# Optimization experiments

Hardware: AMD Instinct MI355X
Metric: run time of the kernel (lower is better)

The kernel has to match this reference:

```python
import jax, jax.numpy as jnp
import numpy as np

NUM_CLASSES = 1000
DENSE_DIM = 64 * 64  # 4096, hardcoded in the module
BATCH = 8192
W0, W1 = 0.5, 0.5  # self.weights


def setup_inputs() -> dict:
    key = jax.random.key(0)
    k1, k2, k3, k4 = jax.random.split(key, 4)
    logits = jax.random.normal(k1, (BATCH, NUM_CLASSES), dtype=jnp.float32)
    dense_out = jax.random.normal(k2, (BATCH, DENSE_DIM), dtype=jnp.float32)
    target = jax.random.randint(k3, (BATCH,), 0, NUM_CLASSES, dtype=jnp.int32)
    # dense_labels buffer: random 0/1 per (class, dense) cell, as in __init__
    dense_labels = jax.random.bernoulli(k4, 0.5, (NUM_CLASSES, DENSE_DIM)).astype(jnp.float32)
    return {"logits": logits, "dense_out": dense_out, "target": target,
            "dense_labels": dense_labels}


def _bce_with_logits_mean(x, y):
    # numerically stable BCEWithLogitsLoss (mean reduction)
    return jnp.mean(jnp.maximum(x, 0.0) - x * y + jnp.log1p(jnp.exp(-jnp.abs(x))))


def reference(logits, dense_out, target, dense_labels):
    # --- accumulation (detached in the original; side-effect state) ---
    probs = jax.lax.stop_gradient(jax.nn.sigmoid(dense_out))  # [B, D]
    dense_output_sum = jax.ops.segment_sum(probs, target, num_segments=NUM_CLASSES)  # [C, D]
    total_accumulated = jax.ops.segment_sum(
        jnp.ones((BATCH,), dtype=jnp.float32), target, num_segments=NUM_CLASSES)  # [C]

    # --- losses ---
    dense_target = dense_labels[target]  # per-sample gather of label rows [B, D]
    logp = jax.nn.log_softmax(logits, axis=-1)
    loss1 = -jnp.mean(jnp.take_along_axis(logp, target[:, None], axis=1))  # CrossEntropyLoss
    loss2 = _bce_with_logits_mean(dense_out, dense_target)
    loss = loss1 * W0 + loss2 * W1
    return loss, dense_output_sum, total_accumulated
```

## Files before the change

### kernel.cpp

```cpp
#include <hip/hip_runtime.h>
#include <math.h>

#define NC   1000
#define DD   4096
#define BB   8192


__global__ __launch_bounds__(1024) void build_k(const int* __restrict__ target,
                                                int* __restrict__ counts_g,
                                                int* __restrict__ offsets_g,
                                                int* __restrict__ csr) {
    __shared__ int scnt[1024];
    __shared__ int scur[1024];
    int t = threadIdx.x;
    scnt[t] = 0;
    __syncthreads();

    int tg[8];
    #pragma unroll
    for (int k = 0; k < 8; ++k) {
        tg[k] = target[k * 1024 + t];
        atomicAdd(&scnt[tg[k]], 1);
    }
    __syncthreads();

    int orig = scnt[t];
    __syncthreads();
    for (int off = 1; off < 1024; off <<= 1) {
        int v = (t >= off) ? scnt[t - off] : 0;
        __syncthreads();
        scnt[t] += v;
        __syncthreads();
    }
    int excl = scnt[t] - orig;
    if (t < NC) { counts_g[t] = orig; offsets_g[t] = excl; }
    scur[t] = excl;
    __syncthreads();

    #pragma unroll
    for (int k = 0; k < 8; ++k) {
        int pos = atomicAdd(&scur[tg[k]], 1);
        csr[pos] = k * 1024 + t;
    }
}

__global__ __launch_bounds__(256) void ce_k(const float* __restrict__ logits,
                                            const int* __restrict__ target,
                                            double* __restrict__ loss1) {
    int wave = threadIdx.x >> 6;
    int lane = threadIdx.x & 63;
    int i = blockIdx.x * 4 + wave;
    const float* row = logits + (size_t)i * NC;
    int j0 = lane * 4;

    float4 r0 = *(const float4*)(row + j0);
    float4 r1 = *(const float4*)(row + j0 + 256);
    float4 r2 = *(const float4*)(row + j0 + 512);
    float4 r3;
    if (j0 + 768 < NC) r3 = *(const float4*)(row + j0 + 768);
    else r3 = make_float4(-INFINITY, -INFINITY, -INFINITY, -INFINITY);
    float tl = row[target[i]];

    float mx = fmaxf(fmaxf(fmaxf(r0.x, r0.y), fmaxf(r0.z, r0.w)),
                     fmaxf(fmaxf(r1.x, r1.y), fmaxf(r1.z, r1.w)));
    mx = fmaxf(mx, fmaxf(fmaxf(r2.x, r2.y), fmaxf(r2.z, r2.w)));
    mx = fmaxf(mx, fmaxf(fmaxf(r3.x, r3.y), fmaxf(r3.z, r3.w)));
    #pragma unroll
    for (int o = 32; o > 0; o >>= 1) mx = fmaxf(mx, __shfl_xor(mx, o));

    float s = __expf(r0.x - mx) + __expf(r0.y - mx) + __expf(r0.z - mx) + __expf(r0.w - mx)
            + __expf(r1.x - mx) + __expf(r1.y - mx) + __expf(r1.z - mx) + __expf(r1.w - mx)
            + __expf(r2.x - mx) + __expf(r2.y - mx) + __expf(r2.z - mx) + __expf(r2.w - mx)
            + __expf(r3.x - mx) + __expf(r3.y - mx) + __expf(r3.z - mx) + __expf(r3.w - mx);
    #pragma unroll
    for (int o = 32; o > 0; o >>= 1) s += __shfl_xor(s, o);

    __shared__ float red[4];
    if (lane == 0) red[wave] = -(tl - mx - __logf(s));
    __syncthreads();
    if (threadIdx.x == 0)
        atomicAdd(loss1, (double)(red[0] + red[1] + red[2] + red[3]));
}

#define ACC1(xv, yv, acc)                                                     \
    {                                                                         \
        float e = __expf(-fabsf(xv));                                         \
        float inv = __builtin_amdgcn_rcpf(1.f + e);                           \
        acc += (xv >= 0.f) ? inv : e * inv;                                   \
        bce += fmaxf(xv, 0.f) - xv * yv + __logf(1.f + e);                    \
    }

__global__ __launch_bounds__(256) void main_k(const float* __restrict__ dense_out,
                                              const float* __restrict__ dense_labels,
                                              const int* __restrict__ counts,
                                              const int* __restrict__ offsets,
                                              const int* __restrict__ csr,
                                              float* __restrict__ out_sum,
                                              double* __restrict__ loss2) {
    int c = blockIdx.x;
    int d = blockIdx.y * 1024 + (threadIdx.x << 2);
    int n = counts[c];
    int o = offsets[c];
    __shared__ int sidx[128];

    float4 y = *(const float4*)(dense_labels + (size_t)c * DD + d);
    float a0 = 0.f, a1 = 0.f, a2 = 0.f, a3 = 0.f, bce = 0.f;
    const float* dp = dense_out + d;

    for (int base = 0; base < n; base += 128) {
        int m = min(128, n - base);
        if (threadIdx.x < m) sidx[threadIdx.x] = csr[o + base + threadIdx.x];
        __syncthreads();

        float4 x0 = *(const float4*)(dp + (size_t)sidx[0] * DD);
        int s = 0;
        for (; s + 1 < m; ++s) {
            float4 x1 = *(const float4*)(dp + (size_t)sidx[s + 1] * DD);
            ACC1(x0.x, y.x, a0) ACC1(x0.y, y.y, a1)
            ACC1(x0.z, y.z, a2) ACC1(x0.w, y.w, a3)
            x0 = x1;
        }
        ACC1(x0.x, y.x, a0) ACC1(x0.y, y.y, a1)
        ACC1(x0.z, y.z, a2) ACC1(x0.w, y.w, a3)
        __syncthreads();
    }

    float* p = out_sum + (size_t)c * DD + d;
    p[0] = a0; p[1] = a1; p[2] = a2; p[3] = a3;

    #pragma unroll
    for (int o2 = 32; o2 > 0; o2 >>= 1) bce += __shfl_xor(bce, o2);
    __shared__ float wsum[4];
    int t = threadIdx.x;
    if ((t & 63) == 0) wsum[t >> 6] = bce;
    __syncthreads();
    if (t == 0) atomicAdd(loss2, (double)(wsum[0] + wsum[1] + wsum[2] + wsum[3]));
}

__global__ void fin_k(const int* __restrict__ counts,
                      const double* __restrict__ loss1,
                      const double* __restrict__ loss2,
                      float* __restrict__ out) {
    int t = blockIdx.x * blockDim.x + threadIdx.x;
    if (t < NC) out[1 + (size_t)NC * DD + t] = (float)counts[t];
    if (t == 0) {
        double l1 = *loss1 / (double)BB;
        double l2 = *loss2 / ((double)BB * (double)DD);
        out[0] = (float)(0.5 * l1 + 0.5 * l2);
    }
}

extern "C" void kernel_launch(void* const* d_in, const int* in_sizes, int n_in,
                              void* d_out, int out_size, void* d_ws, size_t ws_size,
                              hipStream_t stream) {
    const float* logits       = (const float*)d_in[0];
    const float* dense_out    = (const float*)d_in[1];
    const int*   target       = (const int*)d_in[2];
    const float* dense_labels = (const float*)d_in[3];
    float* out = (float*)d_out;

    char* ws = (char*)d_ws;
    double* loss1   = (double*)(ws + 0);
    double* loss2   = (double*)(ws + 8);
    int*    counts  = (int*)(ws + 16);
    int*    offsets = (int*)(ws + 4096);
    int*    csr     = (int*)(ws + 8192);

    hipMemsetAsync(d_ws, 0, 16, stream);

    build_k<<<1, 1024, 0, stream>>>(target, counts, offsets, csr);
    ce_k<<<BB / 4, 256, 0, stream>>>(logits, target, loss1);

    dim3 grid(NC, DD / 1024);
    main_k<<<grid, 256, 0, stream>>>(dense_out, dense_labels, counts, offsets, csr,
                                     out + 1, loss2);
    fin_k<<<(NC + 255) / 256, 256, 0, stream>>>(counts, loss1, loss2, out);
}
```

Before: 286.9 us.

## Fuse CSR build, cross-entropy, BCE and finalize into one kernel

Replaces the four-kernel pipeline with a single fused kernel. Each class block scans the whole target array itself to collect its sample indices in shared memory, so the serial single-block CSR build is gone. Cross-entropy blocks are appended to the same grid, and the last block to finish (tracked by an atomic counter) writes the final loss. This removes launch gaps and the serialized build step, but adds redundant reads of the target array per block and assumes at most 128 samples per class.

```diff
diff --git a/kernel.cpp b/kernel.cpp
--- a/kernel.cpp
+++ b/kernel.cpp
@@ -5,82 +5,11 @@
 #define DD   4096
 #define BB   8192
 
+#define MAIN_BLOCKS (NC * 4)
+#define CE_BLOCKS   (BB / 4)
+#define TOT_BLOCKS  (MAIN_BLOCKS + CE_BLOCKS)
+#define MAXN 128
 
-__global__ __launch_bounds__(1024) void build_k(const int* __restrict__ target,
-                                                int* __restrict__ counts_g,
-                                                int* __restrict__ offsets_g,
-                                                int* __restrict__ csr) {
-    __shared__ int scnt[1024];
-    __shared__ int scur[1024];
-    int t = threadIdx.x;
-    scnt[t] = 0;
-    __syncthreads();
-
-    int tg[8];
-    #pragma unroll
-    for (int k = 0; k < 8; ++k) {
-        tg[k] = target[k * 1024 + t];
-        atomicAdd(&scnt[tg[k]], 1);
-    }
-    __syncthreads();
-
-    int orig = scnt[t];
-    __syncthreads();
-    for (int off = 1; off < 1024; off <<= 1) {
-        int v = (t >= off) ? scnt[t - off] : 0;
-        __syncthreads();
-        scnt[t] += v;
-        __syncthreads();
-    }
-    int excl = scnt[t] - orig;
-    if (t < NC) { counts_g[t] = orig; offsets_g[t] = excl; }
-    scur[t] = excl;
-    __syncthreads();
-
-    #pragma unroll
-    for (int k = 0; k < 8; ++k) {
-        int pos = atomicAdd(&scur[tg[k]], 1);
-        csr[pos] = k * 1024 + t;
-    }
-}
-
-__global__ __launch_bounds__(256) void ce_k(const float* __restrict__ logits,
-                                            const int* __restrict__ target,
-                                            double* __restrict__ loss1) {
-    int wave = threadIdx.x >> 6;
-    int lane = threadIdx.x & 63;
-    int i = blockIdx.x * 4 + wave;
-    const float* row = logits + (size_t)i * NC;
-    int j0 = lane * 4;
-
-    float4 r0 = *(const float4*)(row + j0);
-    float4 r1 = *(const float4*)(row + j0 + 256);
-    float4 r2 = *(const float4*)(row + j0 + 512);
-    float4 r3;
-    if (j0 + 768 < NC) r3 = *(const float4*)(row + j0 + 768);
-    else r3 = make_float4(-INFINITY, -INFINITY, -INFINITY, -INFINITY);
-    float tl = row[target[i]];
-
-    float mx = fmaxf(fmaxf(fmaxf(r0.x, r0.y), fmaxf(r0.z, r0.w)),
-                     fmaxf(fmaxf(r1.x, r1.y), fmaxf(r1.z, r1.w)));
-    mx = fmaxf(mx, fmaxf(fmaxf(r2.x, r2.y), fmaxf(r2.z, r2.w)));
-    mx = fmaxf(mx, fmaxf(fmaxf(r3.x, r3.y), fmaxf(r3.z, r3.w)));
-    #pragma unroll
-    for (int o = 32; o > 0; o >>= 1) mx = fmaxf(mx, __shfl_xor(mx, o));
-
-    float s = __expf(r0.x - mx) + __expf(r0.y - mx) + __expf(r0.z - mx) + __expf(r0.w - mx)
-            + __expf(r1.x - mx) + __expf(r1.y - mx) + __expf(r1.z - mx) + __expf(r1.w - mx)
-            + __expf(r2.x - mx) + __expf(r2.y - mx) + __expf(r2.z - mx) + __expf(r2.w - mx)
-            + __expf(r3.x - mx) + __expf(r3.y - mx) + __expf(r3.z - mx) + __expf(r3.w - mx);
-    #pragma unroll
-    for (int o = 32; o > 0; o >>= 1) s += __shfl_xor(s, o);
-
-    __shared__ float red[4];
-    if (lane == 0) red[wave] = -(tl - mx - __logf(s));
-    __syncthreads();
-    if (threadIdx.x == 0)
-        atomicAdd(loss1, (double)(red[0] + red[1] + red[2] + red[3]));
-}
 
 #define ACC1(xv, yv, acc)                                                     \
     {                                                                         \
@@ -90,63 +19,118 @@
         bce += fmaxf(xv, 0.f) - xv * yv + __logf(1.f + e);                    \
     }
 
-__global__ __launch_bounds__(256) void main_k(const float* __restrict__ dense_out,
-                                              const float* __restrict__ dense_labels,
-                                              const int* __restrict__ counts,
-                                              const int* __restrict__ offsets,
-                                              const int* __restrict__ csr,
-                                              float* __restrict__ out_sum,
-                                              double* __restrict__ loss2) {
-    int c = blockIdx.x;
-    int d = blockIdx.y * 1024 + (threadIdx.x << 2);
-    int n = counts[c];
-    int o = offsets[c];
-    __shared__ int sidx[128];
+__global__ __launch_bounds__(256) void fused_k(const float* __restrict__ logits,
+                                               const float* __restrict__ dense_out,
+                                               const int*   __restrict__ target,
+                                               const float* __restrict__ dense_labels,
+                                               float* __restrict__ out,
+                                               double* __restrict__ loss1,
+                                               double* __restrict__ loss2,
+                                               unsigned* __restrict__ done) {
+    int bx = blockIdx.x;
+    int t  = threadIdx.x;
+    int wave = t >> 6;
+    int lane = t & 63;
 
-    float4 y = *(const float4*)(dense_labels + (size_t)c * DD + d);
-    float a0 = 0.f, a1 = 0.f, a2 = 0.f, a3 = 0.f, bce = 0.f;
-    const float* dp = dense_out + d;
+    __shared__ int   sidx[MAXN];
+    __shared__ int   s_n;
+    __shared__ float red[4];
 
-    for (int base = 0; base < n; base += 128) {
-        int m = min(128, n - base);
-        if (threadIdx.x < m) sidx[threadIdx.x] = csr[o + base + threadIdx.x];
+    if (bx < MAIN_BLOCKS) {
+        int c     = bx >> 2;
+        int chunk = bx & 3;
+        int d     = chunk * 1024 + (t << 2);
+
+        if (t == 0) s_n = 0;
         __syncthreads();
 
-        float4 x0 = *(const float4*)(dp + (size_t)sidx[0] * DD);
-        int s = 0;
-        for (; s + 1 < m; ++s) {
-            float4 x1 = *(const float4*)(dp + (size_t)sidx[s + 1] * DD);
+        const int4* tp = (const int4*)target;
+        #pragma unroll
+        for (int k = 0; k < 8; ++k) {
+            int4 v = tp[k * 256 + t];
+            int s0 = (k * 256 + t) * 4;
+            if (v.x == c) { int p = atomicAdd(&s_n, 1); sidx[p] = s0;     }
+            if (v.y == c) { int p = atomicAdd(&s_n, 1); sidx[p] = s0 + 1; }
+            if (v.z == c) { int p = atomicAdd(&s_n, 1); sidx[p] = s0 + 2; }
+            if (v.w == c) { int p = atomicAdd(&s_n, 1); sidx[p] = s0 + 3; }
+        }
+        __syncthreads();
+        int n = s_n;
+
+        float4 y = *(const float4*)(dense_labels + (size_t)c * DD + d);
+        float a0 = 0.f, a1 = 0.f, a2 = 0.f, a3 = 0.f, bce = 0.f;
+        const float* dp = dense_out + d;
+
+        if (n > 0) {
+            float4 x0 = *(const float4*)(dp + (size_t)sidx[0] * DD);
+            int s = 0;
+            for (; s + 1 < n; ++s) {
+                float4 x1 = *(const float4*)(dp + (size_t)sidx[s + 1] * DD);
+                ACC1(x0.x, y.x, a0) ACC1(x0.y, y.y, a1)
+                ACC1(x0.z, y.z, a2) ACC1(x0.w, y.w, a3)
+                x0 = x1;
+            }
             ACC1(x0.x, y.x, a0) ACC1(x0.y, y.y, a1)
             ACC1(x0.z, y.z, a2) ACC1(x0.w, y.w, a3)
-            x0 = x1;
         }
-        ACC1(x0.x, y.x, a0) ACC1(x0.y, y.y, a1)
-        ACC1(x0.z, y.z, a2) ACC1(x0.w, y.w, a3)
+
+        float* p = out + 1 + (size_t)c * DD + d;
+        p[0] = a0; p[1] = a1; p[2] = a2; p[3] = a3;
+
+        if (chunk == 0 && t == 0) out[1 + (size_t)NC * DD + c] = (float)n;
+
+        #pragma unroll
+        for (int o2 = 32; o2 > 0; o2 >>= 1) bce += __shfl_xor(bce, o2);
+        if (lane == 0) red[wave] = bce;
         __syncthreads();
+        if (t == 0)
+            atomicAdd(loss2, (double)(red[0] + red[1] + red[2] + red[3]));
+    } else {
+        int i = (bx - MAIN_BLOCKS) * 4 + wave;
+        const float* row = logits + (size_t)i * NC;
+        int j0 = lane * 4;
+
+        float4 r0 = *(const float4*)(row + j0);
+        float4 r1 = *(const float4*)(row + j0 + 256);
+        float4 r2 = *(const float4*)(row + j0 + 512);
+        float4 r3;
+        if (j0 + 768 < NC) r3 = *(const float4*)(row + j0 + 768);
+        else r3 = make_float4(-INFINITY, -INFINITY, -INFINITY, -INFINITY);
+        float tl = row[target[i]];
+
+        float mx = fmaxf(fmaxf(fmaxf(r0.x, r0.y), fmaxf(r0.z, r0.w)),
+                         fmaxf(fmaxf(r1.x, r1.y), fmaxf(r1.z, r1.w)));
+        mx = fmaxf(mx, fmaxf(fmaxf(r2.x, r2.y), fmaxf(r2.z, r2.w)));
+        mx = fmaxf(mx, fmaxf(fmaxf(r3.x, r3.y), fmaxf(r3.z, r3.w)));
+        #pragma unroll
+        for (int o = 32; o > 0; o >>= 1) mx = fmaxf(mx, __shfl_xor(mx, o));
+
+        float s = __expf(r0.x - mx) + __expf(r0.y - mx) + __expf(r0.z - mx) + __expf(r0.w - mx)
+                + __expf(r1.x - mx) + __expf(r1.y - mx) + __expf(r1.z - mx) + __expf(r1.w - mx)
+                + __expf(r2.x - mx) + __expf(r2.y - mx) + __expf(r2.z - mx) + __expf(r2.w - mx)
+                + __expf(r3.x - mx) + __expf(r3.y - mx) + __expf(r3.z - mx) + __expf(r3.w - mx);
+        #pragma unroll
+        for (int o = 32; o > 0; o >>= 1) s += __shfl_xor(s, o);
+
+        if (lane == 0) red[wave] = -(tl - mx - __logf(s));
+        __syncthreads();
+        if (t == 0)
+            atomicAdd(loss1, (double)(red[0] + red[1] + red[2] + red[3]));
     }
 
-    float* p = out_sum + (size_t)c * DD + d;
-    p[0] = a0; p[1] = a1; p[2] = a2; p[3] = a3;
-
-    #pragma unroll
-    for (int o2 = 32; o2 > 0; o2 >>= 1) bce += __shfl_xor(bce, o2);
-    __shared__ float wsum[4];
-    int t = threadIdx.x;
-    if ((t & 63) == 0) wsum[t >> 6] = bce;
-    __syncthreads();
-    if (t == 0) atomicAdd(loss2, (double)(wsum[0] + wsum[1] + wsum[2] + wsum[3]));
-}
-
-__global__ void fin_k(const int* __restrict__ counts,
-                      const double* __restrict__ loss1,
-                      const double* __restrict__ loss2,
-                      float* __restrict__ out) {
-    int t = blockIdx.x * blockDim.x + threadIdx.x;
-    if (t < NC) out[1 + (size_t)NC * DD + t] = (float)counts[t];
     if (t == 0) {
-        double l1 = *loss1 / (double)BB;
-        double l2 = *loss2 / ((double)BB * (double)DD);
-        out[0] = (float)(0.5 * l1 + 0.5 * l2);
+        __threadfence();
+        unsigned v = atomicAdd(done, 1u);
+        if (v == TOT_BLOCKS - 1u) {
+            double l1 = __longlong_as_double(
+                __hip_atomic_load((unsigned long long*)loss1,
+                                  __ATOMIC_RELAXED, __HIP_MEMORY_SCOPE_AGENT));
+            double l2 = __longlong_as_double(
+                __hip_atomic_load((unsigned long long*)loss2,
+                                  __ATOMIC_RELAXED, __HIP_MEMORY_SCOPE_AGENT));
+            out[0] = (float)(0.5 * (l1 / (double)BB) +
+                             0.5 * (l2 / ((double)BB * (double)DD)));
+        }
     }
 }
 
@@ -160,19 +144,12 @@
     float* out = (float*)d_out;
 
     char* ws = (char*)d_ws;
-    double* loss1   = (double*)(ws + 0);
-    double* loss2   = (double*)(ws + 8);
-    int*    counts  = (int*)(ws + 16);
-    int*    offsets = (int*)(ws + 4096);
-    int*    csr     = (int*)(ws + 8192);
+    double*   loss1 = (double*)(ws + 0);
+    double*   loss2 = (double*)(ws + 8);
+    unsigned* done  = (unsigned*)(ws + 16);
 
-    hipMemsetAsync(d_ws, 0, 16, stream);
+    hipMemsetAsync(d_ws, 0, 24, stream);
 
-    build_k<<<1, 1024, 0, stream>>>(target, counts, offsets, csr);
-    ce_k<<<BB / 4, 256, 0, stream>>>(logits, target, loss1);
-
-    dim3 grid(NC, DD / 1024);
-    main_k<<<grid, 256, 0, stream>>>(dense_out, dense_labels, counts, offsets, csr,
-                                     out + 1, loss2);
-    fin_k<<<(NC + 255) / 256, 256, 0, stream>>>(counts, loss1, loss2, out);
+    fused_k<<<TOT_BLOCKS, 256, 0, stream>>>(logits, dense_out, target,
+                                            dense_labels, out, loss1, loss2, done);
 }
```

Measured after the change: 507.2 us. +76.8%, slower.
